# Optimization experiments

Measured on AMD Instinct MI355X. Metric: run time of the kernel, lower is better.

Reference implementation:

```python
import jax, jax.numpy as jnp
import numpy as np

NEG = -1e30  # finite stand-in for -inf so grads stay clean
BLANK = 0


def _ctc_single(lp, tgt, il, tl):
    """CTC negative log-likelihood for one example.
    lp: (T, C) log-probs, tgt: (S,) labels, il/tl: scalar lengths."""
    T, C = lp.shape
    S = tgt.shape[0]
    L = 2 * S + 1  # extended label sequence: blank, t0, blank, t1, ...
    s_idx = jnp.arange(L)
    ext = jnp.where(s_idx % 2 == 0, BLANK, tgt[jnp.minimum(s_idx // 2, S - 1)])
    ext_prev2 = jnp.concatenate([jnp.full((2,), -1, ext.dtype), ext[:-2]])
    allow2 = (s_idx % 2 == 1) & (ext != ext_prev2)  # skip transition allowed
    valid = s_idx < 2 * tl + 1  # mask lattice positions beyond this target

    lp_ext = lp[:, ext]  # (T, L) gather of log-probs onto the lattice

    alpha0 = jnp.full((L,), NEG, lp.dtype)
    alpha0 = alpha0.at[0].set(lp_ext[0, 0])
    alpha0 = alpha0.at[1].set(jnp.where(tl > 0, lp_ext[0, 1], NEG))
    alpha0 = jnp.where(valid, alpha0, NEG)

    def step(alpha, lp_t):
        a1 = alpha
        a2 = jnp.concatenate([jnp.full((1,), NEG, alpha.dtype), alpha[:-1]])
        a3 = jnp.where(allow2,
                       jnp.concatenate([jnp.full((2,), NEG, alpha.dtype), alpha[:-2]]),
                       NEG)
        m = jnp.maximum(a1, jnp.maximum(a2, a3))
        lse = m + jnp.log(jnp.exp(a1 - m) + jnp.exp(a2 - m) + jnp.exp(a3 - m))
        new = jnp.where(valid, lse + lp_t, NEG)
        return new, new

    _, alphas = jax.lax.scan(step, alpha0, lp_ext[1:])
    alphas = jnp.concatenate([alpha0[None], alphas], axis=0)  # (T, L)

    a_fin = alphas[il - 1]
    end1 = a_fin[2 * tl]  # final blank
    end2 = jnp.where(tl > 0, a_fin[jnp.maximum(2 * tl - 1, 0)], NEG)  # final label
    m = jnp.maximum(end1, end2)
    ll = m + jnp.log(jnp.exp(end1 - m) + jnp.exp(end2 - m))
    return -ll


def ctc_loss(log_probs, targets, input_lengths, target_lengths):
    # log_probs: (T, N, C); vmap over the batch axis
    losses = jax.vmap(_ctc_single, in_axes=(1, 0, 0, 0))(
        log_probs, targets, input_lengths, target_lengths)
    # zero_infinity=True: zero out non-finite (huge) losses
    losses = jnp.where(losses >= 1e29, 0.0, losses)
    # reduction='mean': per-example loss divided by target length, then batch mean
    denom = jnp.maximum(target_lengths, 1).astype(losses.dtype)
    return jnp.mean(losses / denom)


def setup_inputs() -> dict:
    key = jax.random.key(0)
    k1, k2 = jax.random.split(key)
    T, N, C, S = 512, 32, 5000, 128
    logits = jax.random.normal(k1, (T, N, C), dtype=jnp.float32)
    log_probs = jax.nn.log_softmax(logits, axis=-1)
    # labels in [1, C): blank index 0 must not appear in targets
    targets = jax.random.randint(k2, (N, S), 1, C, dtype=jnp.int32)
    input_lengths = jnp.full((N,), T, dtype=jnp.int32)
    target_lengths = jnp.full((N,), S, dtype=jnp.int32)
    return {"log_probs": log_probs, "targets": targets,
            "input_lengths": input_lengths, "target_lengths": target_lengths}


def reference(log_probs, targets, input_lengths, target_lengths):
    return ctc_loss(log_probs, targets, input_lengths, target_lengths)
```

## Files before the change

### kernel.cpp

```cpp
#include <hip/hip_runtime.h>

#define T_DIM 512
#define N_DIM 32
#define C_DIM 5000
#define S_DIM 128
#define STRIDE_T (N_DIM * C_DIM)

#define TC 64
#define NCHUNK (T_DIM / TC)
#define LDW 132
#define NLOADERS 192
#define NLOAD ((TC * 129) / NLOADERS)

#define NEGF (-1e30f)
#define LOG2E_F 1.4426950408889634f
#define LN2_F 0.6931471805599453f

__device__ __forceinline__ float fexp2(float x) {
#if __has_builtin(__builtin_amdgcn_exp2f)
    return __builtin_amdgcn_exp2f(x);
#else
    return exp2f(x);
#endif
}
__device__ __forceinline__ float flog2(float x) {
#if __has_builtin(__builtin_amdgcn_logf)
    return __builtin_amdgcn_logf(x);
#else
    return log2f(x);
#endif
}

__device__ __forceinline__ float lse2(float a, float b) {
    float m = fmaxf(a, b);
    return m + flog2(fexp2(a - m) + fexp2(b - m));
}
__device__ __forceinline__ float lse3(float a, float b, float c) {
    float m = fmaxf(a, fmaxf(b, c));
    return m + flog2(fexp2(a - m) + fexp2(b - m) + fexp2(c - m));
}

__global__ __launch_bounds__(256, 1) void ctc_fused_kernel(
        const float* __restrict__ lp,
        const int* __restrict__ tgt,
        const int* __restrict__ il,
        const int* __restrict__ tl,
        float* __restrict__ loss_out)
{
    const int n = blockIdx.x;
    const int tid = threadIdx.x;
    const int wid = tid >> 6;
    const int lane = tid & 63;

    const int tlen = tl[n];
    const int ilen = il[n];
    const int* tgn = tgt + n * S_DIM;
    const float* base = lp + (size_t)n * C_DIM;

    __shared__ float buf[2][TC * LDW];
    __shared__ float sh[2];

    int gof[NLOAD];
    int wo[NLOAD];
    if (wid != 0) {
        const int ltid = tid - 64;
#pragma unroll
        for (int j = 0; j < NLOAD; ++j) {
            const int i = ltid + NLOADERS * j;
            const int t = i / 129;
            const int k = i - 129 * t;
            const int cls = (k < 128) ? tgn[k] : 0;
            gof[j] = t * STRIDE_T + cls;
            wo[j] = t * LDW + k;
        }
        float rg[NLOAD];
#pragma unroll
        for (int j = 0; j < NLOAD; ++j) rg[j] = base[(size_t)gof[j]];
#pragma unroll
        for (int j = 0; j < NLOAD; ++j) buf[0][wo[j]] = rg[j];
    }

    const int c1i = 2 * lane;
    const int c3i = 2 * lane + 1;
    bool allow2_1 = false, allow2_3 = false;
    if (wid == 0) {
        const int c1 = tgn[c1i];
        const int c3 = tgn[c3i];
        const int c1prev = (c1i > 0) ? tgn[c1i - 1] : -1;
        allow2_1 = (c1i > 0) && (c1 != c1prev);
        allow2_3 = (c3 != c1);
    }
    const int vmax = 2 * tlen;
    const int sb = lane << 2;
    const bool v0 = (sb    ) <= vmax;
    const bool v1 = (sb + 1) <= vmax;
    const bool v2 = (sb + 2) <= vmax;
    const bool v3 = (sb + 3) <= vmax;
    const bool v4 = (lane == 63) && (256 <= vmax);
    const int e1s = 2 * tlen;
    const int e2s = (2 * tlen - 1 > 0) ? (2 * tlen - 1) : 0;

    float a0 = NEGF, a1 = NEGF, a2 = NEGF, a3 = NEGF, a4 = NEGF;

    __syncthreads();

    for (int cc = 0; cc < NCHUNK; ++cc) {
        if (wid != 0) {
            if (cc + 1 < NCHUNK) {
                const size_t coff = (size_t)(cc + 1) * TC * STRIDE_T;
                const float* bp = base + coff;
                float* dst = buf[(cc + 1) & 1];
                float rg[NLOAD];
#pragma unroll
                for (int j = 0; j < NLOAD; ++j) rg[j] = bp[(size_t)gof[j]];
#pragma unroll
                for (int j = 0; j < NLOAD; ++j) dst[wo[j]] = rg[j];
            }
        } else {
            const float* lb = buf[cc & 1];
            float2 pq = *(const float2*)&lb[0 * LDW + 2 * lane];
            float pbv = lb[0 * LDW + 128];
#pragma unroll 8
            for (int tt = 0; tt < TC; ++tt) {
                const int ttn = (tt + 1 < TC) ? (tt + 1) : tt;
                const float2 pq_n = *(const float2*)&lb[ttn * LDW + 2 * lane];
                const float pbv_n = lb[ttn * LDW + 128];

                const int t = cc * TC + tt;
                const float pb = pbv  * LOG2E_F;
                const float p1 = pq.x * LOG2E_F;
                const float p3 = pq.y * LOG2E_F;

                if (t == 0) {
                    a0 = (lane == 0) ? pb : NEGF;
                    a1 = (lane == 0 && tlen > 0) ? p1 : NEGF;
                    a2 = NEGF; a3 = NEGF; a4 = NEGF;
                    a0 = v0 ? a0 : NEGF;
                    a1 = v1 ? a1 : NEGF;
                } else {
                    float am1 = __shfl_up(a3, 1);
                    if (lane == 0) am1 = NEGF;

                    const float n0 = lse2(a0, am1);
                    const float n1 = allow2_1 ? lse3(a1, a0, am1) : lse2(a1, a0);
                    const float n2 = lse2(a2, a1);
                    const float n3 = allow2_3 ? lse3(a3, a2, a1) : lse2(a3, a2);
                    const float n4 = lse2(a4, a3);

                    a0 = v0 ? (n0 + pb) : NEGF;
                    a1 = v1 ? (n1 + p1) : NEGF;
                    a2 = v2 ? (n2 + pb) : NEGF;
                    a3 = v3 ? (n3 + p3) : NEGF;
                    a4 = v4 ? (n4 + pb) : NEGF;
                }

                if (t == ilen - 1) {
                    if (sb     == e1s) sh[0] = a0;
                    if (sb + 1 == e1s) sh[0] = a1;
                    if (sb + 2 == e1s) sh[0] = a2;
                    if (sb + 3 == e1s) sh[0] = a3;
                    if (lane == 63 && e1s == 256) sh[0] = a4;
                    if (sb     == e2s) sh[1] = a0;
                    if (sb + 1 == e2s) sh[1] = a1;
                    if (sb + 2 == e2s) sh[1] = a2;
                    if (sb + 3 == e2s) sh[1] = a3;
                }

                pq = pq_n; pbv = pbv_n;
            }
        }
        __syncthreads();
    }

    if (tid == 0) {
        const float e1 = sh[0];
        const float e2 = (tlen > 0) ? sh[1] : NEGF;
        const float m = fmaxf(e1, e2);
        const float ll2 = m + flog2(fexp2(e1 - m) + fexp2(e2 - m));
        const float ll = ll2 * LN2_F;
        float loss = -ll;
        if (loss >= 1e29f) loss = 0.f;
        const int denom = (tlen > 1) ? tlen : 1;
        loss_out[n] = loss / (float)denom;
    }
}

__global__ __launch_bounds__(64, 1) void ctc_reduce_kernel(
        const float* __restrict__ loss, float* __restrict__ out)
{
    const int lane = threadIdx.x;
    float v = (lane < N_DIM) ? loss[lane] : 0.f;
#pragma unroll
    for (int off = 32; off > 0; off >>= 1) v += __shfl_down(v, off);
    if (lane == 0) out[0] = v / (float)N_DIM;
}

extern "C" void kernel_launch(void* const* d_in, const int* in_sizes, int n_in,
                              void* d_out, int out_size, void* d_ws, size_t ws_size,
                              hipStream_t stream) {
    const float* lp = (const float*)d_in[0];
    const int* tgt = (const int*)d_in[1];
    const int* il = (const int*)d_in[2];
    const int* tl = (const int*)d_in[3];
    float* out = (float*)d_out;
    float* losses = (float*)d_ws;

    ctc_fused_kernel<<<N_DIM, 256, 0, stream>>>(lp, tgt, il, tl, losses);
    ctc_reduce_kernel<<<1, 64, 0, stream>>>(losses, out);
}
```

Measured before the change: 136.3 us.

## Split gather into a grid-wide pre-pass writing a compact lattice buffer

Adds a separate gather kernel that uses 1024 blocks to pull the per-label log-probs for all batches into a compact workspace array. The scan kernel then streams contiguous float2 rows from that buffer into shared memory instead of doing scattered global gathers from only 32 blocks. This spreads the latency-bound random gather across the whole GPU, at the cost of an extra kernel launch and a write plus re-read of about 8.5 MB of workspace. The old fused kernel is kept as a fallback when the workspace is too small.

```diff
diff --git a/kernel.cpp b/kernel.cpp
--- a/kernel.cpp
+++ b/kernel.cpp
@@ -6,11 +6,18 @@
 #define S_DIM 128
 #define STRIDE_T (N_DIM * C_DIM)
 
+#define CROW 130
+#define TOTAL_G (T_DIM * N_DIM * 129)
+#define GBLK 1024
+#define GTHR 256
+#define GSTRIDE (GBLK * GTHR)
+#define GPT 9
+
 #define TC 64
 #define NCHUNK (T_DIM / TC)
-#define LDW 132
+#define CH2 (TC * (CROW / 2))
 #define NLOADERS 192
-#define NLOAD ((TC * 129) / NLOADERS)
+#define NLOADF2 22
 
 #define NEGF (-1e30f)
 #define LOG2E_F 1.4426950408889634f
@@ -40,8 +47,34 @@
     return m + flog2(fexp2(a - m) + fexp2(b - m) + fexp2(c - m));
 }
 
-__global__ __launch_bounds__(256, 1) void ctc_fused_kernel(
+__global__ __launch_bounds__(GTHR, 4) void ctc_gather_kernel(
         const float* __restrict__ lp,
+        const int* __restrict__ tgt,
+        float* __restrict__ compact)
+{
+    const int tid0 = blockIdx.x * GTHR + threadIdx.x;
+    float vals[GPT];
+    int   outi[GPT];
+#pragma unroll
+    for (int j = 0; j < GPT; ++j) {
+        int i = tid0 + GSTRIDE * j;
+        const int ic = (i < TOTAL_G) ? i : (TOTAL_G - 1);
+        const int q = ic / 129;
+        const int k = ic - q * 129;
+        const int nb = q >> 9;
+        const int t = q & 511;
+        const int cls = (k < 128) ? tgt[nb * S_DIM + k] : 0;
+        vals[j] = lp[(size_t)t * STRIDE_T + nb * C_DIM + cls];
+        outi[j] = (i < TOTAL_G) ? (q * CROW + k) : -1;
+    }
+#pragma unroll
+    for (int j = 0; j < GPT; ++j) {
+        if (outi[j] >= 0) compact[(size_t)outi[j]] = vals[j];
+    }
+}
+
+__global__ __launch_bounds__(256, 1) void ctc_scan_kernel(
+        const float* __restrict__ compact,
         const int* __restrict__ tgt,
         const int* __restrict__ il,
         const int* __restrict__ tl,
@@ -55,29 +88,27 @@
     const int tlen = tl[n];
     const int ilen = il[n];
     const int* tgn = tgt + n * S_DIM;
-    const float* base = lp + (size_t)n * C_DIM;
-
-    __shared__ float buf[2][TC * LDW];
+    const float2* cbase2 = (const float2*)(compact + (size_t)n * T_DIM * CROW);
+
+    __shared__ float buf[2][TC * CROW];
     __shared__ float sh[2];
 
-    int gof[NLOAD];
-    int wo[NLOAD];
     if (wid != 0) {
         const int ltid = tid - 64;
-#pragma unroll
-        for (int j = 0; j < NLOAD; ++j) {
-            const int i = ltid + NLOADERS * j;
-            const int t = i / 129;
-            const int k = i - 129 * t;
-            const int cls = (k < 128) ? tgn[k] : 0;
-            gof[j] = t * STRIDE_T + cls;
-            wo[j] = t * LDW + k;
-        }
-        float rg[NLOAD];
-#pragma unroll
-        for (int j = 0; j < NLOAD; ++j) rg[j] = base[(size_t)gof[j]];
-#pragma unroll
-        for (int j = 0; j < NLOAD; ++j) buf[0][wo[j]] = rg[j];
+        float2* dst2 = (float2*)buf[0];
+        float2 rg[NLOADF2];
+#pragma unroll
+        for (int j = 0; j < NLOADF2; ++j) {
+            int i2 = ltid + NLOADERS * j;
+            if (i2 >= CH2) i2 = CH2 - 1;
+            rg[j] = cbase2[i2];
+        }
+#pragma unroll
+        for (int j = 0; j < NLOADF2; ++j) {
+            int i2 = ltid + NLOADERS * j;
+            if (i2 >= CH2) i2 = CH2 - 1;
+            dst2[i2] = rg[j];
+        }
     }
 
     const int c1i = 2 * lane;
@@ -107,24 +138,32 @@
     for (int cc = 0; cc < NCHUNK; ++cc) {
         if (wid != 0) {
             if (cc + 1 < NCHUNK) {
-                const size_t coff = (size_t)(cc + 1) * TC * STRIDE_T;
-                const float* bp = base + coff;
-                float* dst = buf[(cc + 1) & 1];
-                float rg[NLOAD];
-#pragma unroll
-                for (int j = 0; j < NLOAD; ++j) rg[j] = bp[(size_t)gof[j]];
-#pragma unroll
-                for (int j = 0; j < NLOAD; ++j) dst[wo[j]] = rg[j];
+                const int ltid = tid - 64;
+                const float2* src2 = cbase2 + (size_t)(cc + 1) * CH2;
+                float2* dst2 = (float2*)buf[(cc + 1) & 1];
+                float2 rg[NLOADF2];
+#pragma unroll
+                for (int j = 0; j < NLOADF2; ++j) {
+                    int i2 = ltid + NLOADERS * j;
+                    if (i2 >= CH2) i2 = CH2 - 1;
+                    rg[j] = src2[i2];
+                }
+#pragma unroll
+                for (int j = 0; j < NLOADF2; ++j) {
+                    int i2 = ltid + NLOADERS * j;
+                    if (i2 >= CH2) i2 = CH2 - 1;
+                    dst2[i2] = rg[j];
+                }
             }
         } else {
             const float* lb = buf[cc & 1];
-            float2 pq = *(const float2*)&lb[0 * LDW + 2 * lane];
-            float pbv = lb[0 * LDW + 128];
+            float2 pq = *(const float2*)&lb[0 * CROW + 2 * lane];
+            float pbv = lb[0 * CROW + 128];
 #pragma unroll 8
             for (int tt = 0; tt < TC; ++tt) {
                 const int ttn = (tt + 1 < TC) ? (tt + 1) : tt;
-                const float2 pq_n = *(const float2*)&lb[ttn * LDW + 2 * lane];
-                const float pbv_n = lb[ttn * LDW + 128];
+                const float2 pq_n = *(const float2*)&lb[ttn * CROW + 2 * lane];
+                const float pbv_n = lb[ttn * CROW + 128];
 
                 const int t = cc * TC + tt;
                 const float pb = pbv  * LOG2E_F;
@@ -185,6 +224,131 @@
     }
 }
 
+#define FLDW 132
+#define FNLOADERS 192
+#define FNLOAD ((TC * 129) / FNLOADERS)
+
+__global__ __launch_bounds__(256, 1) void ctc_fused_kernel(
+        const float* __restrict__ lp, const int* __restrict__ tgt,
+        const int* __restrict__ il, const int* __restrict__ tl,
+        float* __restrict__ loss_out)
+{
+    const int n = blockIdx.x;
+    const int tid = threadIdx.x;
+    const int wid = tid >> 6;
+    const int lane = tid & 63;
+    const int tlen = tl[n];
+    const int ilen = il[n];
+    const int* tgn = tgt + n * S_DIM;
+    const float* base = lp + (size_t)n * C_DIM;
+    __shared__ float buf[2][TC * FLDW];
+    __shared__ float sh[2];
+    int gof[FNLOAD]; int wo[FNLOAD];
+    if (wid != 0) {
+        const int ltid = tid - 64;
+#pragma unroll
+        for (int j = 0; j < FNLOAD; ++j) {
+            const int i = ltid + FNLOADERS * j;
+            const int t = i / 129;
+            const int k = i - 129 * t;
+            const int cls = (k < 128) ? tgn[k] : 0;
+            gof[j] = t * STRIDE_T + cls;
+            wo[j] = t * FLDW + k;
+        }
+        float rg[FNLOAD];
+#pragma unroll
+        for (int j = 0; j < FNLOAD; ++j) rg[j] = base[(size_t)gof[j]];
+#pragma unroll
+        for (int j = 0; j < FNLOAD; ++j) buf[0][wo[j]] = rg[j];
+    }
+    const int c1i = 2 * lane;
+    const int c3i = 2 * lane + 1;
+    bool allow2_1 = false, allow2_3 = false;
+    if (wid == 0) {
+        const int c1 = tgn[c1i];
+        const int c3 = tgn[c3i];
+        const int c1prev = (c1i > 0) ? tgn[c1i - 1] : -1;
+        allow2_1 = (c1i > 0) && (c1 != c1prev);
+        allow2_3 = (c3 != c1);
+    }
+    const int vmax = 2 * tlen;
+    const int sb = lane << 2;
+    const bool v0 = (sb) <= vmax, v1 = (sb+1) <= vmax, v2 = (sb+2) <= vmax, v3 = (sb+3) <= vmax;
+    const bool v4 = (lane == 63) && (256 <= vmax);
+    const int e1s = 2 * tlen;
+    const int e2s = (2 * tlen - 1 > 0) ? (2 * tlen - 1) : 0;
+    float a0 = NEGF, a1 = NEGF, a2 = NEGF, a3 = NEGF, a4 = NEGF;
+    __syncthreads();
+    for (int cc = 0; cc < NCHUNK; ++cc) {
+        if (wid != 0) {
+            if (cc + 1 < NCHUNK) {
+                const float* bp = base + (size_t)(cc + 1) * TC * STRIDE_T;
+                float* dst = buf[(cc + 1) & 1];
+                float rg[FNLOAD];
+#pragma unroll
+                for (int j = 0; j < FNLOAD; ++j) rg[j] = bp[(size_t)gof[j]];
+#pragma unroll
+                for (int j = 0; j < FNLOAD; ++j) dst[wo[j]] = rg[j];
+            }
+        } else {
+            const float* lb = buf[cc & 1];
+            float2 pq = *(const float2*)&lb[0 * FLDW + 2 * lane];
+            float pbv = lb[0 * FLDW + 128];
+#pragma unroll 8
+            for (int tt = 0; tt < TC; ++tt) {
+                const int ttn = (tt + 1 < TC) ? (tt + 1) : tt;
+                const float2 pq_n = *(const float2*)&lb[ttn * FLDW + 2 * lane];
+                const float pbv_n = lb[ttn * FLDW + 128];
+                const int t = cc * TC + tt;
+                const float pb = pbv * LOG2E_F, p1 = pq.x * LOG2E_F, p3 = pq.y * LOG2E_F;
+                if (t == 0) {
+                    a0 = (lane == 0) ? pb : NEGF;
+                    a1 = (lane == 0 && tlen > 0) ? p1 : NEGF;
+                    a2 = NEGF; a3 = NEGF; a4 = NEGF;
+                    a0 = v0 ? a0 : NEGF;
+                    a1 = v1 ? a1 : NEGF;
+                } else {
+                    float am1 = __shfl_up(a3, 1);
+                    if (lane == 0) am1 = NEGF;
+                    const float n0 = lse2(a0, am1);
+                    const float n1 = allow2_1 ? lse3(a1, a0, am1) : lse2(a1, a0);
+                    const float n2 = lse2(a2, a1);
+                    const float n3 = allow2_3 ? lse3(a3, a2, a1) : lse2(a3, a2);
+                    const float n4 = lse2(a4, a3);
+                    a0 = v0 ? (n0 + pb) : NEGF;
+                    a1 = v1 ? (n1 + p1) : NEGF;
+                    a2 = v2 ? (n2 + pb) : NEGF;
+                    a3 = v3 ? (n3 + p3) : NEGF;
+                    a4 = v4 ? (n4 + pb) : NEGF;
+                }
+                if (t == ilen - 1) {
+                    if (sb     == e1s) sh[0] = a0;
+                    if (sb + 1 == e1s) sh[0] = a1;
+                    if (sb + 2 == e1s) sh[0] = a2;
+                    if (sb + 3 == e1s) sh[0] = a3;
+                    if (lane == 63 && e1s == 256) sh[0] = a4;
+                    if (sb     == e2s) sh[1] = a0;
+                    if (sb + 1 == e2s) sh[1] = a1;
+                    if (sb + 2 == e2s) sh[1] = a2;
+                    if (sb + 3 == e2s) sh[1] = a3;
+                }
+                pq = pq_n; pbv = pbv_n;
+            }
+        }
+        __syncthreads();
+    }
+    if (tid == 0) {
+        const float e1 = sh[0];
+        const float e2 = (tlen > 0) ? sh[1] : NEGF;
+        const float m = fmaxf(e1, e2);
+        const float ll2 = m + flog2(fexp2(e1 - m) + fexp2(e2 - m));
+        float loss = -(ll2 * LN2_F);
+        if (loss >= 1e29f) loss = 0.f;
+        const int denom = (tlen > 1) ? tlen : 1;
+        loss_out[n] = loss / (float)denom;
+    }
+}
+
 __global__ __launch_bounds__(64, 1) void ctc_reduce_kernel(
         const float* __restrict__ loss, float* __restrict__ out)
 {
@@ -204,7 +368,14 @@
     const int* tl = (const int*)d_in[3];
     float* out = (float*)d_out;
     float* losses = (float*)d_ws;
-
-    ctc_fused_kernel<<<N_DIM, 256, 0, stream>>>(lp, tgt, il, tl, losses);
+    float* compact = (float*)((char*)d_ws + 512);
+
+    const size_t need = 512 + (size_t)N_DIM * T_DIM * CROW * sizeof(float);
+    if (ws_size >= need) {
+        ctc_gather_kernel<<<GBLK, GTHR, 0, stream>>>(lp, tgt, compact);
+        ctc_scan_kernel<<<N_DIM, 256, 0, stream>>>(compact, tgt, il, tl, losses);
+    } else {
+        ctc_fused_kernel<<<N_DIM, 256, 0, stream>>>(lp, tgt, il, tl, losses);
+    }
     ctc_reduce_kernel<<<1, 64, 0, stream>>>(losses, out);
 }
```

Measured after the change: 156.6 us. +14.9%, slower.

## Assign one target class per loader thread and load blanks via shuffle

Applied to the files above, without the earlier changes.

Loader warps drop from three to two, and each loader thread now owns one target class. It gathers that class's log-prob for every timestep of the chunk in batches of 32 register loads, replacing the old flattened index tables. The blank log-probs are loaded straight into the compute warp's registers, one timestep per lane, and broadcast with shuffles instead of going through shared memory. Per-thread index computation and register pressure go down, but loader parallelism is lower and the compute warp now issues its own global loads that may stall it.

```diff
diff --git a/kernel.cpp b/kernel.cpp
--- a/kernel.cpp
+++ b/kernel.cpp
@@ -8,9 +8,8 @@
 
 #define TC 64
 #define NCHUNK (T_DIM / TC)
-#define LDW 132
-#define NLOADERS 192
-#define NLOAD ((TC * 129) / NLOADERS)
+#define FLDW 132
+#define LB 32
 
 #define NEGF (-1e30f)
 #define LOG2E_F 1.4426950408889634f
@@ -30,7 +29,6 @@
     return log2f(x);
 #endif
 }
-
 __device__ __forceinline__ float lse2(float a, float b) {
     float m = fmaxf(a, b);
     return m + flog2(fexp2(a - m) + fexp2(b - m));
@@ -40,7 +38,7 @@
     return m + flog2(fexp2(a - m) + fexp2(b - m) + fexp2(c - m));
 }
 
-__global__ __launch_bounds__(256, 1) void ctc_fused_kernel(
+__global__ __launch_bounds__(192, 1) void ctc_fused_kernel(
         const float* __restrict__ lp,
         const int* __restrict__ tgt,
         const int* __restrict__ il,
@@ -57,33 +55,31 @@
     const int* tgn = tgt + n * S_DIM;
     const float* base = lp + (size_t)n * C_DIM;
 
-    __shared__ float buf[2][TC * LDW];
+    __shared__ float buf[2][TC * FLDW];
     __shared__ float sh[2];
 
-    int gof[NLOAD];
-    int wo[NLOAD];
+    int cls = 0;
     if (wid != 0) {
-        const int ltid = tid - 64;
-#pragma unroll
-        for (int j = 0; j < NLOAD; ++j) {
-            const int i = ltid + NLOADERS * j;
-            const int t = i / 129;
-            const int k = i - 129 * t;
-            const int cls = (k < 128) ? tgn[k] : 0;
-            gof[j] = t * STRIDE_T + cls;
-            wo[j] = t * LDW + k;
+        const int k = tid - 64;
+        cls = tgn[k];
+        const float* cb = base + cls;
+#pragma unroll
+        for (int b = 0; b < TC / LB; ++b) {
+            float rg[LB];
+#pragma unroll
+            for (int j = 0; j < LB; ++j)
+                rg[j] = cb[(size_t)(b * LB + j) * STRIDE_T];
+#pragma unroll
+            for (int j = 0; j < LB; ++j)
+                buf[0][(b * LB + j) * FLDW + k] = rg[j];
         }
-        float rg[NLOAD];
-#pragma unroll
-        for (int j = 0; j < NLOAD; ++j) rg[j] = base[(size_t)gof[j]];
-#pragma unroll
-        for (int j = 0; j < NLOAD; ++j) buf[0][wo[j]] = rg[j];
-    }
-
-    const int c1i = 2 * lane;
-    const int c3i = 2 * lane + 1;
+    }
+
+    float blankv = 0.f;
     bool allow2_1 = false, allow2_3 = false;
     if (wid == 0) {
+        blankv = base[(size_t)lane * STRIDE_T];
+        const int c1i = 2 * lane, c3i = 2 * lane + 1;
         const int c1 = tgn[c1i];
         const int c3 = tgn[c3i];
         const int c1prev = (c1i > 0) ? tgn[c1i - 1] : -1;
@@ -107,24 +103,33 @@
     for (int cc = 0; cc < NCHUNK; ++cc) {
         if (wid != 0) {
             if (cc + 1 < NCHUNK) {
-                const size_t coff = (size_t)(cc + 1) * TC * STRIDE_T;
-                const float* bp = base + coff;
+                const int k = tid - 64;
+                const float* cb = base + (size_t)(cc + 1) * TC * STRIDE_T + cls;
                 float* dst = buf[(cc + 1) & 1];
-                float rg[NLOAD];
-#pragma unroll
-                for (int j = 0; j < NLOAD; ++j) rg[j] = bp[(size_t)gof[j]];
-#pragma unroll
-                for (int j = 0; j < NLOAD; ++j) dst[wo[j]] = rg[j];
+#pragma unroll
+                for (int b = 0; b < TC / LB; ++b) {
+                    float rg[LB];
+#pragma unroll
+                    for (int j = 0; j < LB; ++j)
+                        rg[j] = cb[(size_t)(b * LB + j) * STRIDE_T];
+#pragma unroll
+                    for (int j = 0; j < LB; ++j)
+                        dst[(b * LB + j) * FLDW + k] = rg[j];
+                }
             }
         } else {
             const float* lb = buf[cc & 1];
-            float2 pq = *(const float2*)&lb[0 * LDW + 2 * lane];
-            float pbv = lb[0 * LDW + 128];
+            float blankn = 0.f;
+            if (cc + 1 < NCHUNK)
+                blankn = base[((size_t)(cc + 1) * TC + lane) * STRIDE_T];
+
+            float2 pq = *(const float2*)&lb[2 * lane];
+            float pbv = __shfl(blankv, 0);
 #pragma unroll 8
             for (int tt = 0; tt < TC; ++tt) {
                 const int ttn = (tt + 1 < TC) ? (tt + 1) : tt;
-                const float2 pq_n = *(const float2*)&lb[ttn * LDW + 2 * lane];
-                const float pbv_n = lb[ttn * LDW + 128];
+                const float2 pq_n = *(const float2*)&lb[ttn * FLDW + 2 * lane];
+                const float pbv_n = __shfl(blankv, ttn);
 
                 const int t = cc * TC + tt;
                 const float pb = pbv  * LOG2E_F;
@@ -165,9 +170,9 @@
                     if (sb + 2 == e2s) sh[1] = a2;
                     if (sb + 3 == e2s) sh[1] = a3;
                 }
-
                 pq = pq_n; pbv = pbv_n;
             }
+            blankv = blankn;
         }
         __syncthreads();
     }
@@ -177,8 +182,7 @@
         const float e2 = (tlen > 0) ? sh[1] : NEGF;
         const float m = fmaxf(e1, e2);
         const float ll2 = m + flog2(fexp2(e1 - m) + fexp2(e2 - m));
-        const float ll = ll2 * LN2_F;
-        float loss = -ll;
+        float loss = -(ll2 * LN2_F);
         if (loss >= 1e29f) loss = 0.f;
         const int denom = (tlen > 1) ? tlen : 1;
         loss_out[n] = loss / (float)denom;
@@ -205,6 +209,6 @@
     float* out = (float*)d_out;
     float* losses = (float*)d_ws;
 
-    ctc_fused_kernel<<<N_DIM, 256, 0, stream>>>(lp, tgt, il, tl, losses);
+    ctc_fused_kernel<<<N_DIM, 192, 0, stream>>>(lp, tgt, il, tl, losses);
     ctc_reduce_kernel<<<1, 64, 0, stream>>>(losses, out);
 }
```

Result: no change. 138.3 us (+1.5%).
